# Optimization experiments

Measured on AMD Instinct MI355X. Metric: run time of the kernel, lower is better.

The kernel has to match this reference:

```python
import jax, jax.numpy as jnp
import numpy as np

EPS = 1e-5
SLOPE = 0.2

def _leaky(x):
    return jnp.where(x >= 0, x, SLOPE * x)

def _bn(x, g, b, axes):
    # batch-norm in training mode: biased stats over `axes`, per remaining channel dim
    mu = jnp.mean(x, axis=axes, keepdims=True)
    var = jnp.var(x, axis=axes, keepdims=True)
    shape = [1] * x.ndim
    shape[2 if x.ndim == 5 else 1] = -1
    return (x - mu) * jax.lax.rsqrt(var + EPS) * g.reshape(shape) + b.reshape(shape)

def setup_inputs() -> dict:
    key = jax.random.key(0)
    ks = jax.random.split(key, 6)
    T, B, C, H, W, D = 17, 16, 512, 16, 16, 256
    return {
        "cond": jax.random.normal(ks[0], (B, D), jnp.float32),
        "xbar": jax.random.normal(ks[1], (T, B, C, H, W), jnp.float32),
        "lin_w": jax.random.normal(ks[2], (D, D), jnp.float32) * 0.05,
        "lin_b": jnp.zeros((D,), jnp.float32),
        "bn_s_g": jnp.ones((D,), jnp.float32),
        "bn_s_b": jnp.zeros((D,), jnp.float32),
        "conv1_w": jax.random.normal(ks[3], (C, C), jnp.float32) * 0.05,
        "bn1_g": jnp.ones((C,), jnp.float32),
        "bn1_b": jnp.zeros((C,), jnp.float32),
        "conv2_w": jax.random.normal(ks[4], (C, C + D), jnp.float32) * 0.05,
        "bn2_g": jnp.ones((C,), jnp.float32),
        "bn2_b": jnp.zeros((C,), jnp.float32),
        "conv3_w": jax.random.normal(ks[5], (1, C, 2, 2), jnp.float32) * 0.05,
    }

def reference(cond, xbar, lin_w, lin_b, bn_s_g, bn_s_b, conv1_w, bn1_g, bn1_b, conv2_w, bn2_g, bn2_b, conv3_w):
    # sent_map: Linear -> BatchNorm1d (over batch) -> LeakyReLU
    sent = cond @ lin_w.T + lin_b                       # [B, D]
    sent = _leaky(_bn(sent, bn_s_g, bn_s_b, axes=(0,)))

    motions = xbar[1:] - xbar[:-1]                      # [F, B, C, H, W]
    F, B, C, H, W = motions.shape

    # motion_map: 1x1 conv -> BN (per-frame stats, matching the python loop) -> LeakyReLU
    h = jnp.einsum('fbchw,oc->fbohw', motions, conv1_w)
    h = _leaky(_bn(h, bn1_g, bn1_b, axes=(1, 3, 4)))

    # broadcast sentence vector over space (replaces per-pixel python loop)
    sent_dupe = jnp.broadcast_to(sent[None, :, :, None, None], (F, B, sent.shape[1], H, W))
    ms = jnp.concatenate([h, sent_dupe], axis=2)        # [F, B, C+D, H, W]

    # predictor: 1x1 conv -> BN (per-frame) -> LeakyReLU -> 2x2 stride-2 conv
    h2 = jnp.einsum('fbchw,oc->fbohw', ms, conv2_w)
    h2 = _leaky(_bn(h2, bn2_g, bn2_b, axes=(1, 3, 4)))

    h2f = h2.reshape(F * B, C, H, W)
    out = jax.lax.conv_general_dilated(
        h2f, conv3_w, window_strides=(2, 2), padding='VALID',
        dimension_numbers=('NCHW', 'OIHW', 'NCHW'))     # [F*B, 1, H/2, W/2]
    return out.reshape(F, B, -1)                        # matches view(B,-1) per frame + stack
```

## Files before the change

kernel.cpp:

```cpp
#include <hip/hip_runtime.h>
#include <hip/hip_bf16.h>

#define EPS 1e-5f
#define SLOPE 0.2f

#define NF 16
#define NBATCH 16
#define NC 512
#define NHW 256
#define ND 256
#define K2 768
#define MF 4096
#define FRAME_ELEMS ((size_t)MF * NC)

typedef __attribute__((ext_vector_type(8))) short short8;
typedef __attribute__((ext_vector_type(4))) float float4v;

__device__ __forceinline__ float lrelu(float v) { return v >= 0.f ? v : SLOPE * v; }
__device__ __forceinline__ float b2f(ushort u) { union { float f; uint i; } x; x.i = ((uint)u) << 16; return x.f; }
__device__ __forceinline__ ushort f2b(float f) {
  uint i = __float_as_uint(f);
  return (ushort)((i + 0x7FFFu + ((i >> 16) & 1u)) >> 16);
}
__device__ __forceinline__ void gl16(const ushort* g, ushort* l) {
  __builtin_amdgcn_global_load_lds(
      (const __attribute__((address_space(1))) unsigned int*)g,
      (__attribute__((address_space(3))) unsigned int*)l, 16, 0, 0);
}

__global__ __launch_bounds__(256) void k_sent(
    const float* __restrict__ cond, const float* __restrict__ lin_w,
    const float* __restrict__ lin_b, const float* __restrict__ gam,
    const float* __restrict__ bet, float* __restrict__ sent) {
  int d = threadIdx.x;
  float acc[NBATCH];
  float bias = lin_b[d];
#pragma unroll
  for (int b = 0; b < NBATCH; ++b) acc[b] = bias;
  for (int k = 0; k < ND; ++k) {
    float w = lin_w[d * ND + k];
#pragma unroll
    for (int b = 0; b < NBATCH; ++b) acc[b] = fmaf(cond[b * ND + k], w, acc[b]);
  }
  float mu = 0.f;
#pragma unroll
  for (int b = 0; b < NBATCH; ++b) mu += acc[b];
  mu *= (1.f / NBATCH);
  float var = 0.f;
#pragma unroll
  for (int b = 0; b < NBATCH; ++b) { float t = acc[b] - mu; var = fmaf(t, t, var); }
  var *= (1.f / NBATCH);
  float sc = rsqrtf(var + EPS) * gam[d];
  float sh = bet[d] - mu * sc;
#pragma unroll
  for (int b = 0; b < NBATCH; ++b) sent[b * ND + d] = lrelu(fmaf(acc[b], sc, sh));
}

__global__ __launch_bounds__(256) void k_bias2(
    const float* __restrict__ sent, const float* __restrict__ w2,
    float* __restrict__ bias2) {
  int o = blockIdx.x * 256 + threadIdx.x;
  float acc[NBATCH];
#pragma unroll
  for (int b = 0; b < NBATCH; ++b) acc[b] = 0.f;
  for (int d = 0; d < ND; ++d) {
    float w = w2[(size_t)o * K2 + NC + d];
#pragma unroll
    for (int b = 0; b < NBATCH; ++b) acc[b] = fmaf(sent[b * ND + d], w, acc[b]);
  }
#pragma unroll
  for (int b = 0; b < NBATCH; ++b) bias2[b * NC + o] = acc[b];
}

__global__ __launch_bounds__(256) void k_wcvt(
    const float* __restrict__ w1, const float* __restrict__ w2,
    ushort* __restrict__ w1b, ushort* __restrict__ w2b) {
  int i = blockIdx.x * 256 + threadIdx.x;
  w1b[i] = f2b(w1[i]);
  int o = i >> 9, c = i & 511;
  w2b[i] = f2b(w2[(size_t)o * K2 + c]);
}

__global__ __launch_bounds__(256) void k_mot(
    const float* __restrict__ xbar, ushort* __restrict__ mot, int f0, int nb) {
  __shared__ float T[64][65];
  int b = blockIdx.y;
  int hw0 = (blockIdx.x & 3) * 64;
  int c0 = (blockIdx.x >> 2) * 64;
  int t = threadIdx.x;
  int w = t >> 6, l = t & 63;
  int fs = blockIdx.z * 4;
  int fe = fs + 4 < nb ? fs + 4 : nb;

  const float* xp = xbar + ((size_t)(f0 + fs) * NBATCH + b) * (NC * NHW) + hw0 + l;
  float prev[16];
#pragma unroll
  for (int k = 0; k < 16; ++k) prev[k] = xp[(size_t)(c0 + 4 * k + w) * NHW];

  for (int fr = fs; fr < fe; ++fr) {
    const float* xc = xbar + ((size_t)(f0 + fr + 1) * NBATCH + b) * (NC * NHW) + hw0 + l;
    float cur[16];
#pragma unroll
    for (int k = 0; k < 16; ++k) cur[k] = xc[(size_t)(c0 + 4 * k + w) * NHW];
#pragma unroll
    for (int k = 0; k < 16; ++k) T[4 * k + w][l] = cur[k] - prev[k];
    __syncthreads();
    ushort* mp = mot + ((size_t)fr * MF + b * NHW + hw0) * NC + c0;
#pragma unroll
    for (int k = 0; k < 16; ++k) mp[(size_t)(4 * k + w) * NC + l] = f2b(T[l][4 * k + w]);
    __syncthreads();
#pragma unroll
    for (int k = 0; k < 16; ++k) prev[k] = cur[k];
  }
}

template <int BIAS>
__global__ __launch_bounds__(256) void k_gemm(
    const ushort* __restrict__ A, const ushort* __restrict__ W,
    const float* __restrict__ bias2, ushort* __restrict__ H,
    float2* __restrict__ part) {
  __shared__ ushort lds[2][8192];
  int t = threadIdx.x;
  int w = t >> 6, l = t & 63;
  int g = blockIdx.z;
  int m0 = blockIdx.x * 128;
  int n0 = blockIdx.y * 128;
  int wr = w >> 1, wc = w & 1;

  const ushort* Ag = A + ((size_t)g * MF + m0) * NC;
  const ushort* Wg = W + (size_t)n0 * NC;

  float4v acc[4][4];
#pragma unroll
  for (int i = 0; i < 4; ++i)
#pragma unroll
    for (int j = 0; j < 4; ++j) acc[i][j] = (float4v)0.f;

  int s1 = (w * 2 + 0) * 64 + l;
  int s2 = (w * 2 + 1) * 64 + l;
  size_t ga1 = (size_t)(s1 >> 2) * NC + (s1 & 3) * 8;
  size_t ga2 = (size_t)(s2 >> 2) * NC + (s2 & 3) * 8;

#define STAGE(buf, c0)                                  \
  do {                                                  \
    gl16(Ag + ga1 + (c0), &lds[buf][s1 * 8]);           \
    gl16(Ag + ga2 + (c0), &lds[buf][s2 * 8]);           \
    gl16(Wg + ga1 + (c0), &lds[buf][4096 + s1 * 8]);    \
    gl16(Wg + ga2 + (c0), &lds[buf][4096 + s2 * 8]);    \
  } while (0)

  STAGE(0, 0);
  asm volatile("s_waitcnt vmcnt(0)" ::: "memory");
  __syncthreads();

  for (int kt = 0; kt < 16; ++kt) {
    int cur = kt & 1;
    if (kt < 15) STAGE(cur ^ 1, (kt + 1) * 32);
    short8 af[4], bfr[4];
#pragma unroll
    for (int i = 0; i < 4; ++i)
      af[i] = *(const short8*)&lds[cur][(wr * 64 + i * 16 + (l & 15)) * 32 + (l >> 4) * 8];
#pragma unroll
    for (int j = 0; j < 4; ++j)
      bfr[j] = *(const short8*)&lds[cur][4096 + (wc * 64 + j * 16 + (l & 15)) * 32 + (l >> 4) * 8];
#pragma unroll
    for (int i = 0; i < 4; ++i)
#pragma unroll
      for (int j = 0; j < 4; ++j)
        acc[i][j] = __builtin_amdgcn_mfma_f32_16x16x32_bf16(af[i], bfr[j], acc[i][j], 0, 0, 0);
    if (kt < 15) {
      asm volatile("s_waitcnt vmcnt(0)" ::: "memory");
      __syncthreads();
    }
  }
#undef STAGE
  __syncthreads();

  float bz[4];
#pragma unroll
  for (int fn = 0; fn < 4; ++fn)
    bz[fn] = BIAS ? bias2[(m0 >> 8) * NC + n0 + wc * 64 + fn * 16 + (l & 15)] : 0.f;

  float sv[4], qv[4];
#pragma unroll
  for (int fn = 0; fn < 4; ++fn) {
    float s = 0.f, q = 0.f;
#pragma unroll
    for (int fm = 0; fm < 4; ++fm)
#pragma unroll
      for (int j = 0; j < 4; ++j) {
        float v = acc[fm][fn][j] + bz[fn];
        acc[fm][fn][j] = v;
        s += v;
        q = fmaf(v, v, q);
      }
    s += __shfl_xor(s, 16); s += __shfl_xor(s, 32);
    q += __shfl_xor(q, 16); q += __shfl_xor(q, 32);
    sv[fn] = s; qv[fn] = q;
  }
  if (l < 16) {
    int mb = blockIdx.x * 2 + wr;
    float2* pp = part + ((size_t)g * 64 + mb) * NC + n0 + wc * 64 + l;
#pragma unroll
    for (int fn = 0; fn < 4; ++fn) pp[fn * 16] = make_float2(sv[fn], qv[fn]);
  }

  ushort* ep = &lds[0][w * 1088];
  ushort* Hg = H + ((size_t)g * MF + m0 + wr * 64) * NC + n0 + wc * 64;
#pragma unroll
  for (int fm = 0; fm < 4; ++fm) {
#pragma unroll
    for (int fn = 0; fn < 4; ++fn)
#pragma unroll
      for (int j = 0; j < 4; ++j)
        ep[((l >> 4) * 4 + j) * 68 + fn * 16 + (l & 15)] = f2b(acc[fm][fn][j]);
#pragma unroll
    for (int h = 0; h < 2; ++h) {
      int r = h * 8 + (l >> 3), sl = l & 7;
      short8 v = *(const short8*)&ep[r * 68 + sl * 8];
      *(short8*)&Hg[(size_t)(fm * 16 + r) * NC + sl * 8] = v;
    }
  }
}

__global__ __launch_bounds__(256) void k_stats2(
    const float2* __restrict__ part, const float* __restrict__ gam,
    const float* __restrict__ bet, float2* __restrict__ st) {
  int bi = blockIdx.x;
  int g = bi >> 1;
  int o = (bi & 1) * 256 + threadIdx.x;
  float s = 0.f, q = 0.f;
#pragma unroll
  for (int mb = 0; mb < 64; ++mb) {
    float2 v = part[((size_t)g * 64 + mb) * NC + o];
    s += v.x;
    q += v.y;
  }
  float mu = s * (1.f / 4096.f);
  float var = q * (1.f / 4096.f) - mu * mu;
  float sc = rsqrtf(var + EPS) * gam[o];
  st[g * NC + o] = make_float2(sc, bet[o] - mu * sc);
}

__global__ __launch_bounds__(256) void k_act(
    const ushort* __restrict__ h1, const float2* __restrict__ st,
    ushort* __restrict__ a2) {
  int g = blockIdx.z;
  size_t i0 = ((size_t)blockIdx.x * 256 + threadIdx.x) * 8;
  int o0 = (int)(i0 & 511);
  const ushort* src = h1 + (size_t)g * FRAME_ELEMS + i0;
  ushort* dst = a2 + (size_t)g * FRAME_ELEMS + i0;
  short8 v = *(const short8*)src;
  short8 r;
#pragma unroll
  for (int e = 0; e < 8; ++e) {
    float2 ss = st[g * NC + o0 + e];
    float x = fmaf(b2f((ushort)v[e]), ss.x, ss.y);
    r[e] = (short)f2b(lrelu(x));
  }
  *(short8*)dst = r;
}

__global__ __launch_bounds__(256) void k_conv3(
    const ushort* __restrict__ h2, const float2* __restrict__ st2,
    const float* __restrict__ w3, float* __restrict__ out, int f0) {
  int g = blockIdx.z;
  int b = blockIdx.x;
  int t = threadIdx.x;
  int oi = t >> 2;
  int cs = t & 3;
  int y = oi >> 3, x = oi & 7;
  const ushort* base = h2 + ((size_t)g * MF + b * NHW) * NC;
  int m00 = (2 * y) * 16 + 2 * x;
  float acc = 0.f;
  for (int c8 = cs * 128; c8 < cs * 128 + 128; c8 += 8) {
    short8 v0 = *(const short8*)&base[(size_t)(m00 + 0) * NC + c8];
    short8 v1 = *(const short8*)&base[(size_t)(m00 + 1) * NC + c8];
    short8 v2 = *(const short8*)&base[(size_t)(m00 + 16) * NC + c8];
    short8 v3 = *(const short8*)&base[(size_t)(m00 + 17) * NC + c8];
#pragma unroll
    for (int e = 0; e < 8; ++e) {
      float2 ss = st2[g * NC + c8 + e];
      float4 wv = ((const float4*)w3)[c8 + e];
      acc = fmaf(lrelu(fmaf(b2f((ushort)v0[e]), ss.x, ss.y)), wv.x, acc);
      acc = fmaf(lrelu(fmaf(b2f((ushort)v1[e]), ss.x, ss.y)), wv.y, acc);
      acc = fmaf(lrelu(fmaf(b2f((ushort)v2[e]), ss.x, ss.y)), wv.z, acc);
      acc = fmaf(lrelu(fmaf(b2f((ushort)v3[e]), ss.x, ss.y)), wv.w, acc);
    }
  }
  acc += __shfl_xor(acc, 1);
  acc += __shfl_xor(acc, 2);
  if (cs == 0) out[((size_t)(f0 + g) * NBATCH + b) * 64 + oi] = acc;
}

extern "C" void kernel_launch(void* const* d_in, const int* in_sizes, int n_in,
                              void* d_out, int out_size, void* d_ws, size_t ws_size,
                              hipStream_t stream) {
  const float* cond = (const float*)d_in[0];
  const float* xbar = (const float*)d_in[1];
  const float* lin_w = (const float*)d_in[2];
  const float* lin_b = (const float*)d_in[3];
  const float* bnsg = (const float*)d_in[4];
  const float* bnsb = (const float*)d_in[5];
  const float* w1 = (const float*)d_in[6];
  const float* bn1g = (const float*)d_in[7];
  const float* bn1b = (const float*)d_in[8];
  const float* w2 = (const float*)d_in[9];
  const float* bn2g = (const float*)d_in[10];
  const float* bn2b = (const float*)d_in[11];
  const float* w3 = (const float*)d_in[12];
  float* out = (float*)d_out;

  char* p = (char*)d_ws;
  float* sent = (float*)p;    p += ((NBATCH * ND * 4 + 255) & ~255);
  float* bias2 = (float*)p;   p += ((NBATCH * NC * 4 + 255) & ~255);
  float2* st1 = (float2*)p;   p += ((NF * NC * 8 + 255) & ~255);
  float2* st2 = (float2*)p;   p += ((NF * NC * 8 + 255) & ~255);
  float2* part = (float2*)p;  p += (((size_t)NF * 64 * NC * 8 + 255) & ~255);
  ushort* w1b = (ushort*)p;   p += ((NC * NC * 2 + 255) & ~255);
  ushort* w2b = (ushort*)p;   p += ((NC * NC * 2 + 255) & ~255);
  size_t used = (size_t)(p - (char*)d_ws);
  const size_t frame_bytes = FRAME_ELEMS * 2;
  size_t rem = ws_size > used ? ws_size - used : 0;
  int FB = (int)(rem / (3 * frame_bytes));
  if (FB < 1) FB = 1;
  if (FB > NF) FB = NF;
  ushort* bufA = (ushort*)p;
  ushort* bufB = bufA + (size_t)FB * FRAME_ELEMS;
  ushort* bufC = bufB + (size_t)FB * FRAME_ELEMS;

  k_wcvt<<<1024, 256, 0, stream>>>(w1, w2, w1b, w2b);
  k_sent<<<1, 256, 0, stream>>>(cond, lin_w, lin_b, bnsg, bnsb, sent);
  k_bias2<<<2, 256, 0, stream>>>(sent, w2, bias2);

  for (int f0 = 0; f0 < NF; f0 += FB) {
    int nb = (NF - f0) < FB ? (NF - f0) : FB;
    int ngrp = (nb + 3) / 4;
    k_mot<<<dim3(32, NBATCH, ngrp), 256, 0, stream>>>(xbar, bufA, f0, nb);
    k_gemm<0><<<dim3(32, 4, nb), 256, 0, stream>>>(bufA, w1b, nullptr, bufB, part);
    k_stats2<<<2 * nb, 256, 0, stream>>>(part, bn1g, bn1b, st1);
    k_act<<<dim3(1024, 1, nb), 256, 0, stream>>>(bufB, st1, bufA);
    k_gemm<1><<<dim3(32, 4, nb), 256, 0, stream>>>(bufA, w2b, bias2, bufC, part);
    k_stats2<<<2 * nb, 256, 0, stream>>>(part, bn2g, bn2b, st2);
    k_conv3<<<dim3(NBATCH, 1, nb), 256, 0, stream>>>(bufC, st2, w3, out, f0);
  }
}
```

Before: 306.4 us.

## Load GEMM operands directly to registers and merge the small prep kernels

New measurement: 451.0 us. 1.47x slower.

```diff
diff --git a/kernel.cpp b/kernel.cpp
--- a/kernel.cpp
+++ b/kernel.cpp
@@ -22,17 +22,23 @@
   uint i = __float_as_uint(f);
   return (ushort)((i + 0x7FFFu + ((i >> 16) & 1u)) >> 16);
 }
-__device__ __forceinline__ void gl16(const ushort* g, ushort* l) {
-  __builtin_amdgcn_global_load_lds(
-      (const __attribute__((address_space(1))) unsigned int*)g,
-      (__attribute__((address_space(3))) unsigned int*)l, 16, 0, 0);
-}
-
-__global__ __launch_bounds__(256) void k_sent(
+
+__global__ __launch_bounds__(256) void k_pre(
+    const float* __restrict__ w1, const float* __restrict__ w2,
     const float* __restrict__ cond, const float* __restrict__ lin_w,
     const float* __restrict__ lin_b, const float* __restrict__ gam,
-    const float* __restrict__ bet, float* __restrict__ sent) {
-  int d = threadIdx.x;
+    const float* __restrict__ bet,
+    ushort* __restrict__ w1b, ushort* __restrict__ w2b,
+    float* __restrict__ sent) {
+  int bx = blockIdx.x, t = threadIdx.x;
+  if (bx < 1024) {
+    int i = bx * 256 + t;
+    w1b[i] = f2b(w1[i]);
+    int o = i >> 9, c = i & 511;
+    w2b[i] = f2b(w2[(size_t)o * K2 + c]);
+    return;
+  }
+  int d = t;
   float acc[NBATCH];
   float bias = lin_b[d];
 #pragma unroll
@@ -48,7 +54,7 @@
   mu *= (1.f / NBATCH);
   float var = 0.f;
 #pragma unroll
-  for (int b = 0; b < NBATCH; ++b) { float t = acc[b] - mu; var = fmaf(t, t, var); }
+  for (int b = 0; b < NBATCH; ++b) { float x = acc[b] - mu; var = fmaf(x, x, var); }
   var *= (1.f / NBATCH);
   float sc = rsqrtf(var + EPS) * gam[d];
   float sh = bet[d] - mu * sc;
@@ -56,41 +62,34 @@
   for (int b = 0; b < NBATCH; ++b) sent[b * ND + d] = lrelu(fmaf(acc[b], sc, sh));
 }
 
-__global__ __launch_bounds__(256) void k_bias2(
+__global__ __launch_bounds__(256) void k_mot(
+    const float* __restrict__ xbar, ushort* __restrict__ mot, int f0, int nb,
     const float* __restrict__ sent, const float* __restrict__ w2,
     float* __restrict__ bias2) {
-  int o = blockIdx.x * 256 + threadIdx.x;
-  float acc[NBATCH];
-#pragma unroll
-  for (int b = 0; b < NBATCH; ++b) acc[b] = 0.f;
-  for (int d = 0; d < ND; ++d) {
-    float w = w2[(size_t)o * K2 + NC + d];
-#pragma unroll
-    for (int b = 0; b < NBATCH; ++b) acc[b] = fmaf(sent[b * ND + d], w, acc[b]);
-  }
-#pragma unroll
-  for (int b = 0; b < NBATCH; ++b) bias2[b * NC + o] = acc[b];
-}
-
-__global__ __launch_bounds__(256) void k_wcvt(
-    const float* __restrict__ w1, const float* __restrict__ w2,
-    ushort* __restrict__ w1b, ushort* __restrict__ w2b) {
-  int i = blockIdx.x * 256 + threadIdx.x;
-  w1b[i] = f2b(w1[i]);
-  int o = i >> 9, c = i & 511;
-  w2b[i] = f2b(w2[(size_t)o * K2 + c]);
-}
-
-__global__ __launch_bounds__(256) void k_mot(
-    const float* __restrict__ xbar, ushort* __restrict__ mot, int f0, int nb) {
+  int t = threadIdx.x;
+  if (blockIdx.x == 32) {
+    if (blockIdx.z != 0 || blockIdx.y >= 2) return;
+    int o = blockIdx.y * 256 + t;
+    float acc[NBATCH];
+#pragma unroll
+    for (int b = 0; b < NBATCH; ++b) acc[b] = 0.f;
+    for (int d = 0; d < ND; ++d) {
+      float w = w2[(size_t)o * K2 + NC + d];
+#pragma unroll
+      for (int b = 0; b < NBATCH; ++b) acc[b] = fmaf(sent[b * ND + d], w, acc[b]);
+    }
+#pragma unroll
+    for (int b = 0; b < NBATCH; ++b) bias2[b * NC + o] = acc[b];
+    return;
+  }
+
   __shared__ float T[64][65];
   int b = blockIdx.y;
   int hw0 = (blockIdx.x & 3) * 64;
   int c0 = (blockIdx.x >> 2) * 64;
-  int t = threadIdx.x;
   int w = t >> 6, l = t & 63;
-  int fs = blockIdx.z * 4;
-  int fe = fs + 4 < nb ? fs + 4 : nb;
+  int fs = blockIdx.z * 8;
+  int fe = fs + 8 < nb ? fs + 8 : nb;
 
   const float* xp = xbar + ((size_t)(f0 + fs) * NBATCH + b) * (NC * NHW) + hw0 + l;
   float prev[16];
@@ -115,20 +114,17 @@
 }
 
 template <int BIAS>
-__global__ __launch_bounds__(256) void k_gemm(
+__global__ __launch_bounds__(256, 3) void k_gemmd(
     const ushort* __restrict__ A, const ushort* __restrict__ W,
     const float* __restrict__ bias2, ushort* __restrict__ H,
     float2* __restrict__ part) {
-  __shared__ ushort lds[2][8192];
-  int t = threadIdx.x;
-  int w = t >> 6, l = t & 63;
-  int g = blockIdx.z;
-  int m0 = blockIdx.x * 128;
-  int n0 = blockIdx.y * 128;
-  int wr = w >> 1, wc = w & 1;
-
-  const ushort* Ag = A + ((size_t)g * MF + m0) * NC;
-  const ushort* Wg = W + (size_t)n0 * NC;
+  __shared__ ushort ep_lds[4][1088];
+  int t = threadIdx.x, w = t >> 6, l = t & 63;
+  int g = blockIdx.z, m0 = blockIdx.x * 64, n0 = blockIdx.y * 256 + w * 64;
+  int ar = l & 15, kb = (l >> 4) * 8;
+
+  const ushort* Ag = A + ((size_t)g * MF + m0 + ar) * NC + kb;
+  const ushort* Wg = W + ((size_t)n0 + ar) * NC + kb;
 
   float4v acc[4][4];
 #pragma unroll
@@ -136,50 +132,41 @@
 #pragma unroll
     for (int j = 0; j < 4; ++j) acc[i][j] = (float4v)0.f;
 
-  int s1 = (w * 2 + 0) * 64 + l;
-  int s2 = (w * 2 + 1) * 64 + l;
-  size_t ga1 = (size_t)(s1 >> 2) * NC + (s1 & 3) * 8;
-  size_t ga2 = (size_t)(s2 >> 2) * NC + (s2 & 3) * 8;
-
-#define STAGE(buf, c0)                                  \
-  do {                                                  \
-    gl16(Ag + ga1 + (c0), &lds[buf][s1 * 8]);           \
-    gl16(Ag + ga2 + (c0), &lds[buf][s2 * 8]);           \
-    gl16(Wg + ga1 + (c0), &lds[buf][4096 + s1 * 8]);    \
-    gl16(Wg + ga2 + (c0), &lds[buf][4096 + s2 * 8]);    \
+#define LOADF(aR, bR, c0)                                             \
+  do {                                                                \
+    _Pragma("unroll") for (int i = 0; i < 4; ++i)                     \
+        aR[i] = *(const short8*)&Ag[(size_t)(i * 16) * NC + (c0)];    \
+    _Pragma("unroll") for (int j = 0; j < 4; ++j)                     \
+        bR[j] = *(const short8*)&Wg[(size_t)(j * 16) * NC + (c0)];    \
   } while (0)
 
-  STAGE(0, 0);
-  asm volatile("s_waitcnt vmcnt(0)" ::: "memory");
-  __syncthreads();
-
+#define MFMA_SET(aR, bR)                                              \
+  do {                                                                \
+    _Pragma("unroll") for (int i = 0; i < 4; ++i)                     \
+      _Pragma("unroll") for (int j = 0; j < 4; ++j)                   \
+          acc[i][j] = __builtin_amdgcn_mfma_f32_16x16x32_bf16(        \
+              aR[i], bR[j], acc[i][j], 0, 0, 0);                      \
+  } while (0)
+
+  short8 a0[4], b0[4], a1[4], b1[4];
+  LOADF(a0, b0, 0);
+#pragma unroll
   for (int kt = 0; kt < 16; ++kt) {
-    int cur = kt & 1;
-    if (kt < 15) STAGE(cur ^ 1, (kt + 1) * 32);
-    short8 af[4], bfr[4];
-#pragma unroll
-    for (int i = 0; i < 4; ++i)
-      af[i] = *(const short8*)&lds[cur][(wr * 64 + i * 16 + (l & 15)) * 32 + (l >> 4) * 8];
-#pragma unroll
-    for (int j = 0; j < 4; ++j)
-      bfr[j] = *(const short8*)&lds[cur][4096 + (wc * 64 + j * 16 + (l & 15)) * 32 + (l >> 4) * 8];
-#pragma unroll
-    for (int i = 0; i < 4; ++i)
-#pragma unroll
-      for (int j = 0; j < 4; ++j)
-        acc[i][j] = __builtin_amdgcn_mfma_f32_16x16x32_bf16(af[i], bfr[j], acc[i][j], 0, 0, 0);
-    if (kt < 15) {
-      asm volatile("s_waitcnt vmcnt(0)" ::: "memory");
-      __syncthreads();
+    if ((kt & 1) == 0) {
+      if (kt < 15) LOADF(a1, b1, (kt + 1) * 32);
+      MFMA_SET(a0, b0);
+    } else {
+      if (kt < 15) LOADF(a0, b0, (kt + 1) * 32);
+      MFMA_SET(a1, b1);
     }
   }
-#undef STAGE
-  __syncthreads();
+#undef LOADF
+#undef MFMA_SET
 
   float bz[4];
 #pragma unroll
   for (int fn = 0; fn < 4; ++fn)
-    bz[fn] = BIAS ? bias2[(m0 >> 8) * NC + n0 + wc * 64 + fn * 16 + (l & 15)] : 0.f;
+    bz[fn] = BIAS ? bias2[(m0 >> 8) * NC + n0 + fn * 16 + (l & 15)] : 0.f;
 
   float sv[4], qv[4];
 #pragma unroll
@@ -199,14 +186,14 @@
     sv[fn] = s; qv[fn] = q;
   }
   if (l < 16) {
-    int mb = blockIdx.x * 2 + wr;
-    float2* pp = part + ((size_t)g * 64 + mb) * NC + n0 + wc * 64 + l;
+    int mb = blockIdx.x;
+    float2* pp = part + ((size_t)g * 64 + mb) * NC + n0 + l;
 #pragma unroll
     for (int fn = 0; fn < 4; ++fn) pp[fn * 16] = make_float2(sv[fn], qv[fn]);
   }
 
-  ushort* ep = &lds[0][w * 1088];
-  ushort* Hg = H + ((size_t)g * MF + m0 + wr * 64) * NC + n0 + wc * 64;
+  ushort* ep = &ep_lds[w][0];
+  ushort* Hg = H + ((size_t)g * MF + m0) * NC + n0;
 #pragma unroll
   for (int fm = 0; fm < 4; ++fm) {
 #pragma unroll
@@ -244,12 +231,12 @@
 
 __global__ __launch_bounds__(256) void k_act(
     const ushort* __restrict__ h1, const float2* __restrict__ st,
-    ushort* __restrict__ a2) {
+    ushort* __restrict__ a1) {
   int g = blockIdx.z;
   size_t i0 = ((size_t)blockIdx.x * 256 + threadIdx.x) * 8;
   int o0 = (int)(i0 & 511);
   const ushort* src = h1 + (size_t)g * FRAME_ELEMS + i0;
-  ushort* dst = a2 + (size_t)g * FRAME_ELEMS + i0;
+  ushort* dst = a1 + (size_t)g * FRAME_ELEMS + i0;
   short8 v = *(const short8*)src;
   short8 r;
 #pragma unroll
@@ -329,18 +316,18 @@
   ushort* bufB = bufA + (size_t)FB * FRAME_ELEMS;
   ushort* bufC = bufB + (size_t)FB * FRAME_ELEMS;
 
-  k_wcvt<<<1024, 256, 0, stream>>>(w1, w2, w1b, w2b);
-  k_sent<<<1, 256, 0, stream>>>(cond, lin_w, lin_b, bnsg, bnsb, sent);
-  k_bias2<<<2, 256, 0, stream>>>(sent, w2, bias2);
+  k_pre<<<1025, 256, 0, stream>>>(w1, w2, cond, lin_w, lin_b, bnsg, bnsb,
+                                  w1b, w2b, sent);
 
   for (int f0 = 0; f0 < NF; f0 += FB) {
     int nb = (NF - f0) < FB ? (NF - f0) : FB;
-    int ngrp = (nb + 3) / 4;
-    k_mot<<<dim3(32, NBATCH, ngrp), 256, 0, stream>>>(xbar, bufA, f0, nb);
-    k_gemm<0><<<dim3(32, 4, nb), 256, 0, stream>>>(bufA, w1b, nullptr, bufB, part);
+    int ngrp = (nb + 7) / 8;
+    k_mot<<<dim3(33, NBATCH, ngrp), 256, 0, stream>>>(xbar, bufA, f0, nb,
+                                                      sent, w2, bias2);
+    k_gemmd<0><<<dim3(64, 2, nb), 256, 0, stream>>>(bufA, w1b, nullptr, bufB, part);
     k_stats2<<<2 * nb, 256, 0, stream>>>(part, bn1g, bn1b, st1);
     k_act<<<dim3(1024, 1, nb), 256, 0, stream>>>(bufB, st1, bufA);
-    k_gemm<1><<<dim3(32, 4, nb), 256, 0, stream>>>(bufA, w2b, bias2, bufC, part);
+    k_gemmd<1><<<dim3(64, 2, nb), 256, 0, stream>>>(bufA, w2b, bias2, bufC, part);
     k_stats2<<<2 * nb, 256, 0, stream>>>(part, bn2g, bn2b, st2);
     k_conv3<<<dim3(NBATCH, 1, nb), 256, 0, stream>>>(bufC, st2, w3, out, f0);
   }
```
